# Optimization experiments

Hardware: AMD Instinct MI355X
Metric: run time of the kernel (lower is better)

The kernel has to match this reference:

```python
import jax, jax.numpy as jnp
import numpy as np

BATCH, TOP_K, MAX_LEN, EMB_DIM = 8, 64, 256, 768


def setup_inputs() -> dict:
    key = jax.random.key(0)
    context = jax.random.normal(key, (BATCH, TOP_K, 2, MAX_LEN, EMB_DIM), dtype=jnp.float32)
    return {"context": context}


def reference(context):
    # context: [B, K, 2, L, D]; slice 0 = context tokens, slice 1 = entity tokens
    ctx = context[:, :, 0, :, :]   # [B, K, L, D]
    ent = context[:, :, 1, :, :]   # [B, K, L, D]
    # similarity: for each context token, score against every entity token
    sim = jnp.einsum("bkld,bkmd->bklm", ctx, ent)  # [B, K, L, L]
    idx = jnp.argmax(sim, axis=-1)                 # [B, K, L] hard attention index
    # gather best-matching entity token per context token
    sel = jnp.take_along_axis(ent, idx[..., None], axis=2)  # [B, K, L, D]
    # dot product per token then sum over tokens (sum-of-max score)
    out = jnp.sum(ctx * sel, axis=(-1, -2))        # [B, K]
    return out
```

## Files before the change

kernel.cpp:

```cpp
#include <hip/hip_runtime.h>


#define MAXLEN 256
#define EMB 768
#define BK 64
#define NSTEP (EMB / BK)
#define LSTRIDE 72

typedef __attribute__((ext_vector_type(4))) float f32x4;
typedef __attribute__((ext_vector_type(8))) short short8;
typedef __bf16 bf16x8 __attribute__((ext_vector_type(8)));

__device__ inline unsigned int pack2bf(float a, float b) {
  unsigned int ua = __builtin_bit_cast(unsigned int, a);
  unsigned int ub = __builtin_bit_cast(unsigned int, b);
  ua = (ua + (0x7fffu + ((ua >> 16) & 1u))) >> 16;
  ub = (ub + (0x7fffu + ((ub >> 16) & 1u))) & 0xffff0000u;
  return ua | ub;
}

__device__ inline uint2 pack4bf(float4 v) {
  uint2 r;
  r.x = pack2bf(v.x, v.y);
  r.y = pack2bf(v.z, v.w);
  return r;
}

__global__ __launch_bounds__(512) void som_rowmax_kernel(
    const float* __restrict__ ctx_all, float* __restrict__ out) {
  __shared__ __align__(16) short lsA[2][MAXLEN][LSTRIDE];
  __shared__ __align__(16) short lsB[2][MAXLEN][LSTRIDE];
  __shared__ float red[8];

  const int t    = threadIdx.x;
  const int w    = t >> 6;
  const int lane = t & 63;
  const int qw   = lane >> 4;
  const int lr   = lane & 15;

  const size_t p = blockIdx.x;
  const float* ctx = ctx_all + p * (size_t)(2 * MAXLEN * EMB);
  const float* ent = ctx + (size_t)(MAXLEN * EMB);

  const int srow = t >> 4;
  const int scol = (t & 15) * 4;
  const float* gA = ctx + (size_t)srow * EMB + scol;
  const float* gB = ent + (size_t)srow * EMB + scol;

  f32x4 acc[2][16];
#pragma unroll
  for (int h = 0; h < 2; ++h)
#pragma unroll
    for (int mt = 0; mt < 16; ++mt)
      acc[h][mt] = (f32x4){0.f, 0.f, 0.f, 0.f};

  float4 ra[8], rb[8];

#pragma unroll
  for (int r = 0; r < 8; ++r) {
    ra[r] = *(const float4*)(gA + (size_t)r * (32 * EMB));
    rb[r] = *(const float4*)(gB + (size_t)r * (32 * EMB));
  }
#pragma unroll
  for (int r = 0; r < 8; ++r) {
    const int row = r * 32 + srow;
    *(uint2*)&lsA[0][row][scol] = pack4bf(ra[r]);
    *(uint2*)&lsB[0][row][scol] = pack4bf(rb[r]);
  }
  __syncthreads();

  const int lt0 = 2 * w;
  const int lt1 = 2 * w + 1;

  for (int step = 0; step < NSTEP; ++step) {
    const int cur = step & 1;

    if (step + 1 < NSTEP) {
      const int k1 = (step + 1) * BK;
#pragma unroll
      for (int r = 0; r < 8; ++r) {
        ra[r] = *(const float4*)(gA + (size_t)r * (32 * EMB) + k1);
        rb[r] = *(const float4*)(gB + (size_t)r * (32 * EMB) + k1);
      }
    }

#pragma unroll
    for (int kh = 0; kh < 2; ++kh) {
      const int kq = kh * 32 + qw * 8;
      bf16x8 a0 = __builtin_bit_cast(bf16x8, *(const short8*)&lsA[cur][lt0 * 16 + lr][kq]);
      bf16x8 a1 = __builtin_bit_cast(bf16x8, *(const short8*)&lsA[cur][lt1 * 16 + lr][kq]);
#pragma unroll
      for (int mt = 0; mt < 16; ++mt) {
        bf16x8 bfr = __builtin_bit_cast(bf16x8, *(const short8*)&lsB[cur][mt * 16 + lr][kq]);
        acc[0][mt] = __builtin_amdgcn_mfma_f32_16x16x32_bf16(a0, bfr, acc[0][mt], 0, 0, 0);
        acc[1][mt] = __builtin_amdgcn_mfma_f32_16x16x32_bf16(a1, bfr, acc[1][mt], 0, 0, 0);
      }
    }

    if (step + 1 < NSTEP) {
#pragma unroll
      for (int r = 0; r < 8; ++r) {
        const int row = r * 32 + srow;
        *(uint2*)&lsA[cur ^ 1][row][scol] = pack4bf(ra[r]);
        *(uint2*)&lsB[cur ^ 1][row][scol] = pack4bf(rb[r]);
      }
    }
    __syncthreads();
  }

  float s = 0.f;
#pragma unroll
  for (int h = 0; h < 2; ++h) {
#pragma unroll
    for (int i = 0; i < 4; ++i) {
      float m = acc[h][0][i];
#pragma unroll
      for (int mt = 1; mt < 16; ++mt) m = fmaxf(m, acc[h][mt][i]);
#pragma unroll
      for (int d = 1; d < 16; d <<= 1) m = fmaxf(m, __shfl_xor(m, d, 64));
      s += m;
    }
  }
  s += __shfl_xor(s, 16, 64);
  s += __shfl_xor(s, 32, 64);

  if (lane == 0) red[w] = s;
  __syncthreads();
  if (t == 0) {
    float tot = 0.f;
#pragma unroll
    for (int i = 0; i < 8; ++i) tot += red[i];
    out[p] = tot;
  }
}

extern "C" void kernel_launch(void* const* d_in, const int* in_sizes, int n_in,
                              void* d_out, int out_size, void* d_ws, size_t ws_size,
                              hipStream_t stream) {
  const float* ctx_all = (const float*)d_in[0];
  float* out = (float*)d_out;
  som_rowmax_kernel<<<dim3(512), dim3(512), 0, stream>>>(ctx_all, out);
}
```

Baseline: 159.3 us.

## Load A fragments directly from global into registers, drop A shared buffer

The context-side MFMA operands are now read straight from global memory in fragment layout and packed to bf16 in registers, so the A tile no longer goes through LDS. Only the entity tile stays double-buffered in shared memory, roughly halving LDS use. Launch bounds request 2 blocks per CU so all 512 blocks can be resident at once. The loop is restructured into a software pipeline with a custom barrier that waits only on LDS counters. The risk is register pressure: 128 accumulator registers plus the prefetch buffers may spill under the tighter occupancy bound.

Result: faster. 150.6 us (-5.5%).

```diff
diff --git a/kernel.cpp b/kernel.cpp
--- a/kernel.cpp
+++ b/kernel.cpp
@@ -4,7 +4,7 @@
 #define MAXLEN 256
 #define EMB 768
 #define BK 64
-#define NSTEP (EMB / BK)
+#define NSTEP 12
 #define LSTRIDE 72
 
 typedef __attribute__((ext_vector_type(4))) float f32x4;
@@ -26,9 +26,17 @@
   return r;
 }
 
-__global__ __launch_bounds__(512) void som_rowmax_kernel(
+__device__ inline bf16x8 pack8bf(float4 a, float4 b) {
+  union { unsigned int u[4]; bf16x8 v; } r;
+  r.u[0] = pack2bf(a.x, a.y);
+  r.u[1] = pack2bf(a.z, a.w);
+  r.u[2] = pack2bf(b.x, b.y);
+  r.u[3] = pack2bf(b.z, b.w);
+  return r.v;
+}
+
+__global__ __launch_bounds__(512, 2) void som_rowmax_kernel(
     const float* __restrict__ ctx_all, float* __restrict__ out) {
-  __shared__ __align__(16) short lsA[2][MAXLEN][LSTRIDE];
   __shared__ __align__(16) short lsB[2][MAXLEN][LSTRIDE];
   __shared__ float red[8];
 
@@ -44,8 +52,11 @@
 
   const int srow = t >> 4;
   const int scol = (t & 15) * 4;
-  const float* gA = ctx + (size_t)srow * EMB + scol;
   const float* gB = ent + (size_t)srow * EMB + scol;
+
+  const int lt0 = 2 * w, lt1 = 2 * w + 1;
+  const float* gA0 = ctx + (size_t)(lt0 * 16 + lr) * EMB + qw * 8;
+  const float* gA1 = ctx + (size_t)(lt1 * 16 + lr) * EMB + qw * 8;
 
   f32x4 acc[2][16];
 #pragma unroll
@@ -54,59 +65,78 @@
     for (int mt = 0; mt < 16; ++mt)
       acc[h][mt] = (f32x4){0.f, 0.f, 0.f, 0.f};
 
-  float4 ra[8], rb[8];
+  float4 rb[8];
+  float4 raA[8];
+  bf16x8 afr[2][2];
 
+  auto issueB = [&](int s) {
 #pragma unroll
-  for (int r = 0; r < 8; ++r) {
-    ra[r] = *(const float4*)(gA + (size_t)r * (32 * EMB));
-    rb[r] = *(const float4*)(gB + (size_t)r * (32 * EMB));
-  }
+    for (int r = 0; r < 8; ++r)
+      rb[r] = *(const float4*)(gB + (size_t)r * (32 * EMB) + s * BK);
+  };
+  auto commitB = [&](int buf) {
 #pragma unroll
-  for (int r = 0; r < 8; ++r) {
-    const int row = r * 32 + srow;
-    *(uint2*)&lsA[0][row][scol] = pack4bf(ra[r]);
-    *(uint2*)&lsB[0][row][scol] = pack4bf(rb[r]);
-  }
-  __syncthreads();
-
-  const int lt0 = 2 * w;
-  const int lt1 = 2 * w + 1;
-
-  for (int step = 0; step < NSTEP; ++step) {
-    const int cur = step & 1;
-
-    if (step + 1 < NSTEP) {
-      const int k1 = (step + 1) * BK;
+    for (int r = 0; r < 8; ++r) {
+      const int row = r * 32 + srow;
+      *(uint2*)&lsB[buf][row][scol] = pack4bf(rb[r]);
+    }
+  };
+  auto issueA = [&](int s) {
 #pragma unroll
-      for (int r = 0; r < 8; ++r) {
-        ra[r] = *(const float4*)(gA + (size_t)r * (32 * EMB) + k1);
-        rb[r] = *(const float4*)(gB + (size_t)r * (32 * EMB) + k1);
+    for (int kh = 0; kh < 2; ++kh)
+#pragma unroll
+      for (int half = 0; half < 2; ++half) {
+        raA[0 * 4 + kh * 2 + half] = *(const float4*)(gA0 + s * BK + kh * 32 + half * 4);
+        raA[1 * 4 + kh * 2 + half] = *(const float4*)(gA1 + s * BK + kh * 32 + half * 4);
       }
-    }
-
+  };
+  auto packA = [&]() {
+#pragma unroll
+    for (int tile = 0; tile < 2; ++tile)
+#pragma unroll
+      for (int kh = 0; kh < 2; ++kh)
+        afr[tile][kh] = pack8bf(raA[tile * 4 + kh * 2 + 0], raA[tile * 4 + kh * 2 + 1]);
+  };
+  auto mfmaStep = [&](int buf) {
 #pragma unroll
     for (int kh = 0; kh < 2; ++kh) {
       const int kq = kh * 32 + qw * 8;
-      bf16x8 a0 = __builtin_bit_cast(bf16x8, *(const short8*)&lsA[cur][lt0 * 16 + lr][kq]);
-      bf16x8 a1 = __builtin_bit_cast(bf16x8, *(const short8*)&lsA[cur][lt1 * 16 + lr][kq]);
 #pragma unroll
       for (int mt = 0; mt < 16; ++mt) {
-        bf16x8 bfr = __builtin_bit_cast(bf16x8, *(const short8*)&lsB[cur][mt * 16 + lr][kq]);
-        acc[0][mt] = __builtin_amdgcn_mfma_f32_16x16x32_bf16(a0, bfr, acc[0][mt], 0, 0, 0);
-        acc[1][mt] = __builtin_amdgcn_mfma_f32_16x16x32_bf16(a1, bfr, acc[1][mt], 0, 0, 0);
+        bf16x8 bfr = __builtin_bit_cast(bf16x8, *(const short8*)&lsB[buf][mt * 16 + lr][kq]);
+        acc[0][mt] = __builtin_amdgcn_mfma_f32_16x16x32_bf16(afr[0][kh], bfr, acc[0][mt], 0, 0, 0);
+        acc[1][mt] = __builtin_amdgcn_mfma_f32_16x16x32_bf16(afr[1][kh], bfr, acc[1][mt], 0, 0, 0);
       }
     }
+  };
+  auto barrier = [&]() {
+    asm volatile("s_waitcnt lgkmcnt(0)" ::: "memory");
+    __builtin_amdgcn_sched_barrier(0);
+    __builtin_amdgcn_s_barrier();
+    __builtin_amdgcn_sched_barrier(0);
+  };
 
-    if (step + 1 < NSTEP) {
-#pragma unroll
-      for (int r = 0; r < 8; ++r) {
-        const int row = r * 32 + srow;
-        *(uint2*)&lsA[cur ^ 1][row][scol] = pack4bf(ra[r]);
-        *(uint2*)&lsB[cur ^ 1][row][scol] = pack4bf(rb[r]);
-      }
-    }
-    __syncthreads();
+  issueB(0);
+  issueA(0);
+  commitB(0);
+  issueB(1);
+  packA();
+  barrier();
+
+  for (int s = 0; s < NSTEP - 2; ++s) {
+    issueA(s + 1);
+    commitB((s + 1) & 1);
+    issueB(s + 2);
+    mfmaStep(s & 1);
+    packA();
+    barrier();
   }
+  issueA(NSTEP - 1);
+  commitB((NSTEP - 1) & 1);
+  mfmaStep((NSTEP - 2) & 1);
+  packA();
+  barrier();
+  mfmaStep((NSTEP - 1) & 1);
 
   float s = 0.f;
 #pragma unroll
```
